# Kernel tuning notes

Measured on AMD Instinct MI355X. Metric: run time of the kernel, lower is better.

The kernel has to match this reference:

```python
import jax, jax.numpy as jnp
import numpy as np

N_NUM = 2048      # recurrent neurons (== input_num)
E_NUM = 1638
OUT_NUM = 512     # readout size
TIME_CONST = 0.1  # LIF leak


def setup_inputs() -> dict:
    key = jax.random.key(0)
    k1, k2, k3, k4, k5 = jax.random.split(key, 5)
    B = 4096
    return {
        "i_": jax.random.normal(k1, (B, N_NUM), dtype=jnp.float32),
        "x": jax.random.normal(k2, (B, N_NUM), dtype=jnp.float32),
        "r": jax.random.normal(k3, (N_NUM, N_NUM), dtype=jnp.float32) * (1.0 / np.sqrt(N_NUM)),
        "f": jax.random.normal(k4, (N_NUM, OUT_NUM), dtype=jnp.float32) * (1.0 / np.sqrt(N_NUM)),
        "b": jax.random.normal(k5, (N_NUM,), dtype=jnp.float32) * 0.01,
    }


def reference(i_, x, r, f, b):
    # EI sign vector: ei_mask is a diagonal matrix diag(signs); mm(ei_mask, A) == signs[:, None] * A
    signs = jnp.where(jnp.arange(N_NUM) < E_NUM, 1.0, -1.0).astype(i_.dtype)
    self_mask = 1.0 - jnp.eye(N_NUM, dtype=i_.dtype)  # no_self: zero diagonal

    # LIF state update: x <- (1 - tau) * x + tau * (i_ + b)   (noise_coeff = 0)
    x_new = (1.0 - TIME_CONST) * x + TIME_CONST * (i_ + b)
    u = jax.nn.relu(x_new)

    # Dale's law + self-mask on recurrent weights; Dale on feedforward weights
    r_eff = signs[:, None] * jnp.abs(r * self_mask)   # [N, N]
    f_eff = signs[:, None] * jnp.abs(f)               # [N, OUT]

    f_out = u @ f_eff   # [B, OUT]
    r_out = u @ r_eff   # [B, N]
    return (f_out, r_out, u)
```

## Files before the change

kernel.cpp:

```cpp
#include <hip/hip_runtime.h>
#include <hip/hip_bf16.h>

#define B_NUM 4096
#define N_NUM 2048
#define E_NUM 1638
#define OUT_NUM 512
#define NTOT 2560
#define KDIM 2048
#define NKT 32

typedef unsigned short u16;
typedef __attribute__((ext_vector_type(8))) __bf16 bf16x8;
typedef __attribute__((ext_vector_type(4))) float f32x4;

__device__ __forceinline__ u16 f2bf(float f) {
  union { float f; unsigned u; } v; v.f = f;
  unsigned r = v.u + 0x7fffu + ((v.u >> 16) & 1u);
  return (u16)(r >> 16);
}

__device__ __forceinline__ void gload16(const u16* src, u16* dst) {
  __builtin_amdgcn_global_load_lds((__attribute__((address_space(1))) void*)src,
                                   (__attribute__((address_space(3))) void*)dst,
                                   16, 0, 0);
}

#define BAR() do { asm volatile("" ::: "memory"); \
                   __builtin_amdgcn_s_barrier();  \
                   asm volatile("" ::: "memory"); } while (0)

__global__ __launch_bounds__(256) void prep_u(const float* __restrict__ in_i,
                                              const float* __restrict__ in_x,
                                              const float* __restrict__ bias,
                                              float* __restrict__ u_f32,
                                              u16* __restrict__ u_bf16) {
  const int t = blockIdx.x * 256 + threadIdx.x;
  const int e = t * 4;
  const float4 iv = *(const float4*)(in_i + e);
  const float4 xv = *(const float4*)(in_x + e);
  const float4 bv = *(const float4*)(bias + (e & (N_NUM - 1)));
  float4 u;
  u.x = fmaxf(0.f, 0.9f * xv.x + 0.1f * (iv.x + bv.x));
  u.y = fmaxf(0.f, 0.9f * xv.y + 0.1f * (iv.y + bv.y));
  u.z = fmaxf(0.f, 0.9f * xv.z + 0.1f * (iv.z + bv.z));
  u.w = fmaxf(0.f, 0.9f * xv.w + 0.1f * (iv.w + bv.w));
  *(float4*)(u_f32 + e) = u;
  ushort4 ub;
  ub.x = f2bf(u.x); ub.y = f2bf(u.y); ub.z = f2bf(u.z); ub.w = f2bf(u.w);
  *(ushort4*)(u_bf16 + e) = ub;
}

__global__ __launch_bounds__(256) void prep_w(const float* __restrict__ r,
                                              const float* __restrict__ f,
                                              u16* __restrict__ wt) {
  __shared__ u16 ldsT[64][72];
  const int k0 = blockIdx.y * 64;
  const int n0 = blockIdx.x * 64;
  const int tid = threadIdx.x;
  const int rloc = tid >> 4;
  const int c4 = (tid & 15) * 4;
#pragma unroll
  for (int rr = 0; rr < 4; ++rr) {
    const int kl = rr * 16 + rloc;
    const int k = k0 + kl;
    const float sign = (k < E_NUM) ? 1.f : -1.f;
    float4 v;
    if (n0 < N_NUM) v = *(const float4*)(r + k * N_NUM + n0 + c4);
    else            v = *(const float4*)(f + k * OUT_NUM + (n0 - N_NUM) + c4);
    float vals[4] = {v.x, v.y, v.z, v.w};
#pragma unroll
    for (int j = 0; j < 4; ++j) {
      float val = sign * fabsf(vals[j]);
      if (n0 < N_NUM && (n0 + c4 + j) == k) val = 0.f;
      ldsT[c4 + j][kl] = f2bf(val);
    }
  }
  __syncthreads();
  const int nl = tid >> 2;
  const int kc = (tid & 3) * 16;
  u16* dst = wt + (n0 + nl) * KDIM + k0 + kc;
  *(uint4*)(dst) = *(const uint4*)&ldsT[nl][kc];
  *(uint4*)(dst + 8) = *(const uint4*)&ldsT[nl][kc + 8];
}

__global__ __launch_bounds__(512, 2) void gemm8(const u16* __restrict__ U,
                                                const u16* __restrict__ Wt,
                                                float* __restrict__ out) {
  __shared__ u16 lds[2][2][256 * 64];
  const int t = threadIdx.x;
  const int w = t >> 6, lane = t & 63;
  const int lr = lane & 15, lg = lane >> 4;
  const int wm = w >> 2, wn = w & 3;
  const int row0 = blockIdx.y * 256;
  const int col0 = blockIdx.x * 256;

  const int srow = t >> 3;
  const int koff = 8 * ((t & 7) ^ (srow & 7));
  const u16* aS = U  + (row0 + srow) * KDIM + koff;
  const u16* bS = Wt + (col0 + srow) * KDIM + koff;
  const int stBase = (w * 8) * 64;

  const int arow = wm * 128 + lr;
  const int brow = wn * 64 + lr;
  const int xs = (lr & 7) << 4;
  const int ca0 = ((lg * 16) ^ xs) >> 1;
  const int ca1 = ((64 + lg * 16) ^ xs) >> 1;

  f32x4 acc[8][4] = {};

#define STAGE_A(c, kt) { const int k0_ = (kt) * 64;                         \
  _Pragma("unroll") for (int i_ = 0; i_ < 4; ++i_)                          \
    gload16(aS + i_ * 64 * KDIM + k0_, &lds[c][0][i_ * 4096 + stBase]); }
#define STAGE_B(c, kt) { const int k0_ = (kt) * 64;                         \
  _Pragma("unroll") for (int i_ = 0; i_ < 4; ++i_)                          \
    gload16(bS + i_ * 64 * KDIM + k0_, &lds[c][1][i_ * 4096 + stBase]); }

  STAGE_B(0, 0);
  STAGE_A(0, 0);
  STAGE_B(1, 1);
  asm volatile("s_waitcnt vmcnt(4)" ::: "memory");
  __builtin_amdgcn_sched_barrier(0);
  BAR();

  for (int T = 0; T < NKT; ++T) {
    const int c = T & 1;
    const u16* lA = lds[c][0];
    const u16* lB = lds[c][1];
    bf16x8 bf[4][2], af[4][2];
#pragma unroll
    for (int ni = 0; ni < 4; ++ni) {
      bf[ni][0] = *(const bf16x8*)&lB[(brow + ni * 16) * 64 + ca0];
      bf[ni][1] = *(const bf16x8*)&lB[(brow + ni * 16) * 64 + ca1];
    }
#pragma unroll
    for (int mi = 0; mi < 4; ++mi) {
      af[mi][0] = *(const bf16x8*)&lA[(arow + mi * 16) * 64 + ca0];
      af[mi][1] = *(const bf16x8*)&lA[(arow + mi * 16) * 64 + ca1];
    }
    { const int tn = (T + 1 < NKT) ? T + 1 : NKT - 1;
      STAGE_A(c ^ 1, tn); }
    BAR();
    __builtin_amdgcn_s_setprio(1);
#pragma unroll
    for (int mi = 0; mi < 4; ++mi)
#pragma unroll
      for (int ni = 0; ni < 4; ++ni) {
        acc[mi][ni] = __builtin_amdgcn_mfma_f32_16x16x32_bf16(af[mi][0], bf[ni][0], acc[mi][ni], 0, 0, 0);
        acc[mi][ni] = __builtin_amdgcn_mfma_f32_16x16x32_bf16(af[mi][1], bf[ni][1], acc[mi][ni], 0, 0, 0);
      }
    __builtin_amdgcn_s_setprio(0);
    BAR();
#pragma unroll
    for (int mi = 0; mi < 4; ++mi) {
      af[mi][0] = *(const bf16x8*)&lA[(arow + 64 + mi * 16) * 64 + ca0];
      af[mi][1] = *(const bf16x8*)&lA[(arow + 64 + mi * 16) * 64 + ca1];
    }
    { const int tn = (T + 2 < NKT) ? T + 2 : NKT - 1;
      STAGE_B(c, tn); }
    BAR();
    __builtin_amdgcn_s_setprio(1);
#pragma unroll
    for (int mi = 0; mi < 4; ++mi)
#pragma unroll
      for (int ni = 0; ni < 4; ++ni) {
        acc[4 + mi][ni] = __builtin_amdgcn_mfma_f32_16x16x32_bf16(af[mi][0], bf[ni][0], acc[4 + mi][ni], 0, 0, 0);
        acc[4 + mi][ni] = __builtin_amdgcn_mfma_f32_16x16x32_bf16(af[mi][1], bf[ni][1], acc[4 + mi][ni], 0, 0, 0);
      }
    __builtin_amdgcn_s_setprio(0);
    asm volatile("s_waitcnt vmcnt(4)" ::: "memory");
    __builtin_amdgcn_sched_barrier(0);
    BAR();
  }
  asm volatile("s_waitcnt vmcnt(0)" ::: "memory");

  const int orow = row0 + wm * 128 + lg * 4;
  const int ocol = col0 + wn * 64 + lr;
  if (col0 < N_NUM) {
    float* ro = out + B_NUM * OUT_NUM;
#pragma unroll
    for (int mi = 0; mi < 8; ++mi)
#pragma unroll
      for (int ni = 0; ni < 4; ++ni)
#pragma unroll
        for (int q = 0; q < 4; ++q)
          ro[(orow + mi * 16 + q) * N_NUM + ocol + ni * 16] = acc[mi][ni][q];
  } else {
#pragma unroll
    for (int mi = 0; mi < 8; ++mi)
#pragma unroll
      for (int ni = 0; ni < 4; ++ni)
#pragma unroll
        for (int q = 0; q < 4; ++q)
          out[(orow + mi * 16 + q) * OUT_NUM + (ocol - N_NUM) + ni * 16] = acc[mi][ni][q];
  }
#undef STAGE_A
#undef STAGE_B
}

extern "C" void kernel_launch(void* const* d_in, const int* in_sizes, int n_in,
                              void* d_out, int out_size, void* d_ws, size_t ws_size,
                              hipStream_t stream) {
  const float* i_ = (const float*)d_in[0];
  const float* x  = (const float*)d_in[1];
  const float* r  = (const float*)d_in[2];
  const float* f  = (const float*)d_in[3];
  const float* b  = (const float*)d_in[4];
  float* out = (float*)d_out;

  u16* U  = (u16*)d_ws;
  u16* Wt = (u16*)((char*)d_ws + (size_t)B_NUM * KDIM * 2);

  float* u_region = out + (size_t)B_NUM * OUT_NUM + (size_t)B_NUM * N_NUM;

  prep_u<<<(B_NUM * N_NUM / 4) / 256, 256, 0, stream>>>(i_, x, b, u_region, U);
  prep_w<<<dim3(NTOT / 64, N_NUM / 64), 256, 0, stream>>>(r, f, Wt);
  gemm8<<<dim3(NTOT / 256, B_NUM / 256), 512, 0, stream>>>(U, Wt, out);
}
```

Measured before the change: 204.3 us.

## Restructure GEMM main loop into quarter-tile phases with finer-grained staging

```diff
diff --git a/kernel.cpp b/kernel.cpp
--- a/kernel.cpp
+++ b/kernel.cpp
@@ -83,93 +83,88 @@
   *(uint4*)(dst + 8) = *(const uint4*)&ldsT[nl][kc + 8];
 }
 
-__global__ __launch_bounds__(512, 2) void gemm8(const u16* __restrict__ U,
-                                                const u16* __restrict__ Wt,
-                                                float* __restrict__ out) {
-  __shared__ u16 lds[2][2][256 * 64];
+__global__ __launch_bounds__(512, 2) void gemm8q(const u16* __restrict__ U,
+                                                 const u16* __restrict__ Wt,
+                                                 float* __restrict__ out) {
+  __shared__ u16 lds[2][2][2][128 * 64];
   const int t = threadIdx.x;
   const int w = t >> 6, lane = t & 63;
   const int lr = lane & 15, lg = lane >> 4;
   const int wm = w >> 2, wn = w & 3;
+  const int hB = wn >> 1;
   const int row0 = blockIdx.y * 256;
   const int col0 = blockIdx.x * 256;
 
-  const int srow = t >> 3;
-  const int koff = 8 * ((t & 7) ^ (srow & 7));
-  const u16* aS = U  + (row0 + srow) * KDIM + koff;
-  const u16* bS = Wt + (col0 + srow) * KDIM + koff;
-  const int stBase = (w * 8) * 64;
-
-  const int arow = wm * 128 + lr;
-  const int brow = wn * 64 + lr;
+  const int sg = w * 8 + (lane >> 3);
+  const int koff = 8 * ((lane & 7) ^ (lane >> 3));
+  const u16* aBase = U + (row0 + sg) * KDIM + koff;
+  const u16* bBase = Wt + (col0 + sg) * KDIM + koff;
+
   const int xs = (lr & 7) << 4;
   const int ca0 = ((lg * 16) ^ xs) >> 1;
   const int ca1 = ((64 + lg * 16) ^ xs) >> 1;
 
   f32x4 acc[8][4] = {};
-
-#define STAGE_A(c, kt) { const int k0_ = (kt) * 64;                         \
-  _Pragma("unroll") for (int i_ = 0; i_ < 4; ++i_)                          \
-    gload16(aS + i_ * 64 * KDIM + k0_, &lds[c][0][i_ * 4096 + stBase]); }
-#define STAGE_B(c, kt) { const int k0_ = (kt) * 64;                         \
-  _Pragma("unroll") for (int i_ = 0; i_ < 4; ++i_)                          \
-    gload16(bS + i_ * 64 * KDIM + k0_, &lds[c][1][i_ * 4096 + stBase]); }
-
-  STAGE_B(0, 0);
-  STAGE_A(0, 0);
-  STAGE_B(1, 1);
-  asm volatile("s_waitcnt vmcnt(4)" ::: "memory");
-  __builtin_amdgcn_sched_barrier(0);
+  bf16x8 af[4][2], b0[2][2], b1[2][2];
+
+#define STA(c, h, kt) { const u16* g_ = aBase + (h) * 128 * KDIM + (kt) * 64;  \
+  gload16(g_,             &lds[c][0][h][w * 512]);                             \
+  gload16(g_ + 64 * KDIM, &lds[c][0][h][(w + 8) * 512]); }
+#define STB(c, h, kt) { const u16* g_ = bBase + (h) * 128 * KDIM + (kt) * 64;  \
+  gload16(g_,             &lds[c][1][h][w * 512]);                             \
+  gload16(g_ + 64 * KDIM, &lds[c][1][h][(w + 8) * 512]); }
+#define RD_A(c, mq) { _Pragma("unroll") for (int mi = 0; mi < 4; ++mi) {       \
+    const int R_ = ((mq) * 64 + mi * 16 + lr) * 64;                            \
+    af[mi][0] = *(const bf16x8*)&lds[c][0][wm][R_ + ca0];                      \
+    af[mi][1] = *(const bf16x8*)&lds[c][0][wm][R_ + ca1]; } }
+#define RD_B(c, dst, nq) { _Pragma("unroll") for (int ni = 0; ni < 2; ++ni) {  \
+    const int R_ = ((wn & 1) * 64 + ((nq) * 2 + ni) * 16 + lr) * 64;           \
+    dst[ni][0] = *(const bf16x8*)&lds[c][1][hB][R_ + ca0];                     \
+    dst[ni][1] = *(const bf16x8*)&lds[c][1][hB][R_ + ca1]; } }
+#define QMFMA(MQ, NQ, bX) { __builtin_amdgcn_s_setprio(1);                     \
+  _Pragma("unroll") for (int mi = 0; mi < 4; ++mi)                             \
+    _Pragma("unroll") for (int ni = 0; ni < 2; ++ni) {                         \
+      acc[(MQ)*4+mi][(NQ)*2+ni] = __builtin_amdgcn_mfma_f32_16x16x32_bf16(     \
+          af[mi][0], bX[ni][0], acc[(MQ)*4+mi][(NQ)*2+ni], 0, 0, 0);           \
+      acc[(MQ)*4+mi][(NQ)*2+ni] = __builtin_amdgcn_mfma_f32_16x16x32_bf16(     \
+          af[mi][1], bX[ni][1], acc[(MQ)*4+mi][(NQ)*2+ni], 0, 0, 0); }         \
+  __builtin_amdgcn_s_setprio(0); }
+#define FENCE4() do { asm volatile("s_waitcnt vmcnt(4)" ::: "memory");         \
+                      __builtin_amdgcn_sched_barrier(0); } while (0)
+
+  STA(0, 0, 0); STA(0, 1, 0); STB(0, 0, 0); STB(0, 1, 0);
+  STB(1, 0, 1); STB(1, 1, 1);
+  FENCE4();
   BAR();
 
-  for (int T = 0; T < NKT; ++T) {
-    const int c = T & 1;
-    const u16* lA = lds[c][0];
-    const u16* lB = lds[c][1];
-    bf16x8 bf[4][2], af[4][2];
-#pragma unroll
-    for (int ni = 0; ni < 4; ++ni) {
-      bf[ni][0] = *(const bf16x8*)&lB[(brow + ni * 16) * 64 + ca0];
-      bf[ni][1] = *(const bf16x8*)&lB[(brow + ni * 16) * 64 + ca1];
-    }
-#pragma unroll
-    for (int mi = 0; mi < 4; ++mi) {
-      af[mi][0] = *(const bf16x8*)&lA[(arow + mi * 16) * 64 + ca0];
-      af[mi][1] = *(const bf16x8*)&lA[(arow + mi * 16) * 64 + ca1];
-    }
-    { const int tn = (T + 1 < NKT) ? T + 1 : NKT - 1;
-      STAGE_A(c ^ 1, tn); }
-    BAR();
-    __builtin_amdgcn_s_setprio(1);
-#pragma unroll
-    for (int mi = 0; mi < 4; ++mi)
-#pragma unroll
-      for (int ni = 0; ni < 4; ++ni) {
-        acc[mi][ni] = __builtin_amdgcn_mfma_f32_16x16x32_bf16(af[mi][0], bf[ni][0], acc[mi][ni], 0, 0, 0);
-        acc[mi][ni] = __builtin_amdgcn_mfma_f32_16x16x32_bf16(af[mi][1], bf[ni][1], acc[mi][ni], 0, 0, 0);
-      }
-    __builtin_amdgcn_s_setprio(0);
-    BAR();
-#pragma unroll
-    for (int mi = 0; mi < 4; ++mi) {
-      af[mi][0] = *(const bf16x8*)&lA[(arow + 64 + mi * 16) * 64 + ca0];
-      af[mi][1] = *(const bf16x8*)&lA[(arow + 64 + mi * 16) * 64 + ca1];
-    }
-    { const int tn = (T + 2 < NKT) ? T + 2 : NKT - 1;
-      STAGE_B(c, tn); }
-    BAR();
-    __builtin_amdgcn_s_setprio(1);
-#pragma unroll
-    for (int mi = 0; mi < 4; ++mi)
-#pragma unroll
-      for (int ni = 0; ni < 4; ++ni) {
-        acc[4 + mi][ni] = __builtin_amdgcn_mfma_f32_16x16x32_bf16(af[mi][0], bf[ni][0], acc[4 + mi][ni], 0, 0, 0);
-        acc[4 + mi][ni] = __builtin_amdgcn_mfma_f32_16x16x32_bf16(af[mi][1], bf[ni][1], acc[4 + mi][ni], 0, 0, 0);
-      }
-    __builtin_amdgcn_s_setprio(0);
-    asm volatile("s_waitcnt vmcnt(4)" ::: "memory");
-    __builtin_amdgcn_sched_barrier(0);
-    BAR();
+  for (int it = 0; it < NKT / 2; ++it) {
+    const int T = 2 * it;
+    const int Tc2 = (T + 2 < NKT) ? T + 2 : NKT - 1;
+    const int Tc3 = (T + 3 < NKT) ? T + 3 : NKT - 1;
+    RD_A(0, 0); RD_B(0, b0, 0);
+    STA(1, 0, T + 1);
+    BAR(); QMFMA(0, 0, b0); BAR();
+    RD_B(0, b1, 1);
+    STA(1, 1, T + 1);
+    BAR(); QMFMA(0, 1, b1); BAR();
+    RD_A(0, 1);
+    STB(0, 0, Tc2);
+    BAR(); QMFMA(1, 0, b0); BAR();
+    STB(0, 1, Tc2);
+    BAR(); QMFMA(1, 1, b1);
+    FENCE4(); BAR();
+    RD_A(1, 0); RD_B(1, b0, 0);
+    STA(0, 0, Tc2);
+    BAR(); QMFMA(0, 0, b0); BAR();
+    RD_B(1, b1, 1);
+    STA(0, 1, Tc2);
+    BAR(); QMFMA(0, 1, b1); BAR();
+    RD_A(1, 1);
+    STB(1, 0, Tc3);
+    BAR(); QMFMA(1, 0, b0); BAR();
+    STB(1, 1, Tc3);
+    BAR(); QMFMA(1, 1, b1);
+    FENCE4(); BAR();
   }
   asm volatile("s_waitcnt vmcnt(0)" ::: "memory");
 
@@ -193,8 +188,12 @@
         for (int q = 0; q < 4; ++q)
           out[(orow + mi * 16 + q) * OUT_NUM + (ocol - N_NUM) + ni * 16] = acc[mi][ni][q];
   }
-#undef STAGE_A
-#undef STAGE_B
+#undef STA
+#undef STB
+#undef RD_A
+#undef RD_B
+#undef QMFMA
+#undef FENCE4
 }
 
 extern "C" void kernel_launch(void* const* d_in, const int* in_sizes, int n_in,
@@ -214,5 +213,5 @@
 
   prep_u<<<(B_NUM * N_NUM / 4) / 256, 256, 0, stream>>>(i_, x, b, u_region, U);
   prep_w<<<dim3(NTOT / 64, N_NUM / 64), 256, 0, stream>>>(r, f, Wt);
-  gemm8<<<dim3(NTOT / 256, B_NUM / 256), 512, 0, stream>>>(U, Wt, out);
-}
+  gemm8q<<<dim3(NTOT / 256, B_NUM / 256), 512, 0, stream>>>(U, Wt, out);
+}
```

Measured after the change: 201.5 us. About the same (-1.4%).
